# Optimization experiments

Hardware: AMD Instinct MI355X
Metric: run time of the kernel (lower is better)

The kernel has to match this reference:

```python
import jax, jax.numpy as jnp
import numpy as np


def setup_inputs() -> dict:
    key = jax.random.key(0)
    k1, k2, k3 = jax.random.split(key, 3)
    B, C, H, W = 16, 512, 64, 64
    K = 32
    std = 1.0 / (K * C) ** 0.5
    x = jax.random.normal(k1, (B, C, H, W), dtype=jnp.float32)
    codewords = jax.random.uniform(k2, (K, C), dtype=jnp.float32, minval=-std, maxval=std)
    scale = jax.random.uniform(k3, (K,), dtype=jnp.float32, minval=-1.0, maxval=0.0)
    return {"x": x, "codewords": codewords, "scale": scale}


def reference(x, codewords, scale):
    # x: [B, C, H, W] -> tokens [B, N, C] with N = H*W
    B, C, H, W = x.shape
    xf = x.reshape(B, C, H * W).transpose(0, 2, 1)  # [B, N, C]

    # (avoids materializing the [B, N, K, C] tensor the torch code builds)
    x_sq = jnp.sum(xf * xf, axis=-1)                 # [B, N]
    c_sq = jnp.sum(codewords * codewords, axis=-1)   # [K]
    xc = jnp.einsum('bnc,kc->bnk', xf, codewords)    # [B, N, K]
    scaled_l2 = scale * (x_sq[..., None] - 2.0 * xc + c_sq)  # [B, N, K]

    w = jax.nn.softmax(scaled_l2, axis=2)            # [B, N, K]

    # aggregate: sum_n w[b,n,k] * (x[b,n,:] - c[k,:])
    #          = einsum(w, x) - (sum_n w) * c
    enc = jnp.einsum('bnk,bnc->bkc', w, xf) - jnp.sum(w, axis=1)[..., None] * codewords
    return enc  # [B, K, C]
```

## Files before the change

### kernel.cpp

```cpp
#include <hip/hip_runtime.h>
#include <hip/hip_bf16.h>


#define B_ 16
#define C_ 512
#define N_ 4096
#define K_ 32
#define XCPAD 40

typedef __attribute__((ext_vector_type(8))) short short8;
typedef __attribute__((ext_vector_type(16))) float floatx16;

__device__ inline unsigned short f2bf(float f) {
    union { float f; unsigned u; } v; v.f = f;
    unsigned r = v.u + 0x7FFFu + ((v.u >> 16) & 1u);
    return (unsigned short)(r >> 16);
}

__global__ __launch_bounds__(256, 2)
void enc_kernel(const float* __restrict__ x, const float* __restrict__ cw,
                const float* __restrict__ scale, float* __restrict__ out)
{
    __shared__ unsigned short XC[C_ * XCPAD];
    __shared__ float Spart[4][32][33];
    __shared__ unsigned short Wl[K_ * XCPAD];
    __shared__ float xsqp[4][32];
    __shared__ float csq[K_];
    __shared__ float scl[K_];
    __shared__ float wsumL[K_];

    const int tid  = threadIdx.x;
    const int wave = tid >> 6;
    const int lane = tid & 63;
    const int l31  = lane & 31;
    const int lh   = lane >> 5;

    const int b     = blockIdx.x >> 5;
    const int chunk = blockIdx.x & 31;
    const long xbase = (long)b * C_ * N_;

    if (tid < K_) scl[tid] = scale[tid];
    {
        const int k = tid >> 3, p = tid & 7;
        const float4* cwr = (const float4*)(cw + k * C_ + p * 64);
        float s = 0.f;
        #pragma unroll
        for (int i = 0; i < 16; ++i) {
            float4 v = cwr[i];
            s += v.x*v.x + v.y*v.y + v.z*v.z + v.w*v.w;
        }
        s += __shfl_xor(s, 1); s += __shfl_xor(s, 2); s += __shfl_xor(s, 4);
        if (p == 0) csq[k] = s;
    }

    short8 cwf[8];
    #pragma unroll
    for (int s = 0; s < 8; ++s) {
        const float* p = cw + l31 * C_ + wave * 128 + s * 16 + lh * 8;
        short8 f;
        #pragma unroll
        for (int j = 0; j < 8; ++j) f[j] = (short)f2bf(p[j]);
        cwf[s] = f;
    }

    floatx16 acc[4];
    floatx16 accW;
    #pragma unroll
    for (int t = 0; t < 4; ++t)
        #pragma unroll
        for (int i = 0; i < 16; ++i) acc[t][i] = 0.f;
    #pragma unroll
    for (int i = 0; i < 16; ++i) accW[i] = 0.f;

    __syncthreads();

    for (int g = 0; g < 4; ++g) {
        const int n0 = chunk * 128 + g * 32;

        {
            const int c0 = tid >> 3;
            const int nq = tid & 7;
            float sq0 = 0.f, sq1 = 0.f, sq2 = 0.f, sq3 = 0.f;
            #pragma unroll
            for (int it = 0; it < 16; ++it) {
                const int c = c0 + 32 * it;
                const float4 v = *(const float4*)(x + xbase + (long)c * N_ + n0 + nq * 4);
                sq0 += v.x*v.x; sq1 += v.y*v.y; sq2 += v.z*v.z; sq3 += v.w*v.w;
                const unsigned lo = (unsigned)f2bf(v.x) | ((unsigned)f2bf(v.y) << 16);
                const unsigned hi = (unsigned)f2bf(v.z) | ((unsigned)f2bf(v.w) << 16);
                *(uint2*)&XC[c * XCPAD + nq * 4] = make_uint2(lo, hi);
            }
            #pragma unroll
            for (int m = 8; m <= 32; m <<= 1) {
                sq0 += __shfl_xor(sq0, m); sq1 += __shfl_xor(sq1, m);
                sq2 += __shfl_xor(sq2, m); sq3 += __shfl_xor(sq3, m);
            }
            if (((tid >> 3) & 7) == 0) {
                xsqp[wave][nq * 4 + 0] = sq0; xsqp[wave][nq * 4 + 1] = sq1;
                xsqp[wave][nq * 4 + 2] = sq2; xsqp[wave][nq * 4 + 3] = sq3;
            }
        }
        __syncthreads();

        {
            floatx16 S;
            #pragma unroll
            for (int i = 0; i < 16; ++i) S[i] = 0.f;
            #pragma unroll
            for (int s = 0; s < 8; ++s) {
                const int cb = wave * 128 + s * 16 + lh * 8;
                short8 a;
                #pragma unroll
                for (int j = 0; j < 8; ++j)
                    a[j] = (short)XC[(cb + j) * XCPAD + l31];
                S = __builtin_amdgcn_mfma_f32_32x32x16_bf16(a, cwf[s], S, 0, 0, 0);
            }
            #pragma unroll
            for (int r = 0; r < 16; ++r) {
                const int n = (r & 3) + 8 * (r >> 2) + 4 * lh;
                Spart[wave][n][l31] = S[r];
            }
        }
        __syncthreads();

        {
            const int n  = tid >> 3;
            const int kq = tid & 7;
            const float xq = xsqp[0][n] + xsqp[1][n] + xsqp[2][n] + xsqp[3][n];
            float L[4];
            #pragma unroll
            for (int i = 0; i < 4; ++i) {
                const int k = kq * 4 + i;
                const float s2 = Spart[0][n][k] + Spart[1][n][k]
                               + Spart[2][n][k] + Spart[3][n][k];
                L[i] = scl[k] * (xq - 2.f * s2 + csq[k]);
            }
            float m = fmaxf(fmaxf(L[0], L[1]), fmaxf(L[2], L[3]));
            m = fmaxf(m, __shfl_xor(m, 1));
            m = fmaxf(m, __shfl_xor(m, 2));
            m = fmaxf(m, __shfl_xor(m, 4));
            float e[4], sum = 0.f;
            #pragma unroll
            for (int i = 0; i < 4; ++i) { e[i] = __expf(L[i] - m); sum += e[i]; }
            sum += __shfl_xor(sum, 1); sum += __shfl_xor(sum, 2); sum += __shfl_xor(sum, 4);
            const float inv = 1.f / sum;
            #pragma unroll
            for (int i = 0; i < 4; ++i)
                Wl[(kq * 4 + i) * XCPAD + n] = f2bf(e[i] * inv);
        }
        __syncthreads();

        {
            short8 aw[2];
            #pragma unroll
            for (int sub = 0; sub < 2; ++sub)
                aw[sub] = *(const short8*)&Wl[l31 * XCPAD + sub * 16 + lh * 8];
            #pragma unroll
            for (int t4 = 0; t4 < 4; ++t4) {
                const int crow = (wave * 4 + t4) * 32 + l31;
                #pragma unroll
                for (int sub = 0; sub < 2; ++sub) {
                    const short8 bx = *(const short8*)&XC[crow * XCPAD + sub * 16 + lh * 8];
                    acc[t4] = __builtin_amdgcn_mfma_f32_32x32x16_bf16(aw[sub], bx, acc[t4], 0, 0, 0);
                }
            }
            if (wave == 0) {
                short8 ones;
                #pragma unroll
                for (int j = 0; j < 8; ++j) ones[j] = (short)0x3F80;
                #pragma unroll
                for (int sub = 0; sub < 2; ++sub)
                    accW = __builtin_amdgcn_mfma_f32_32x32x16_bf16(aw[sub], ones, accW, 0, 0, 0);
            }
        }
        __syncthreads();
    }

    if (wave == 0 && l31 == 0) {
        #pragma unroll
        for (int r = 0; r < 16; ++r) {
            const int k = (r & 3) + 8 * (r >> 2) + 4 * lh;
            wsumL[k] = accW[r];
        }
    }
    __syncthreads();

    #pragma unroll
    for (int t4 = 0; t4 < 4; ++t4) {
        const int c = (wave * 4 + t4) * 32 + l31;
        #pragma unroll
        for (int r = 0; r < 16; ++r) {
            const int k = (r & 3) + 8 * (r >> 2) + 4 * lh;
            const float val = acc[t4][r] - wsumL[k] * cw[k * C_ + c];
            atomicAdd(out + ((b * K_ + k) * C_ + c), val);
        }
    }
}

extern "C" void kernel_launch(void* const* d_in, const int* in_sizes, int n_in,
                              void* d_out, int out_size, void* d_ws, size_t ws_size,
                              hipStream_t stream) {
    const float* x     = (const float*)d_in[0];
    const float* cw    = (const float*)d_in[1];
    const float* scale = (const float*)d_in[2];
    float* out = (float*)d_out;
    hipMemsetAsync(out, 0, (size_t)out_size * sizeof(float), stream);
    hipLaunchKernelGGL(enc_kernel, dim3(B_ * 32), dim3(256), 0, stream,
                       x, cw, scale, out);
}
```

Measured before the change: 230.4 us.

## Double-buffer x loads, shrink LDS partials, and replace output atomics with workspace reduce

Global loads of x are now software-pipelined across channel quarters and groups using two register buffers, so memory latency overlaps the bf16 conversion. The per-wave Spart partials are merged through LDS atomics into a single tile, and launch bounds are raised to 3 blocks per CU. The ones-MFMA row sum is replaced by a scalar sum of the bf16 weights. When enough workspace exists, each block writes its partial result plainly and a second kernel sums the 32 chunks, replacing the memset and global atomics. The cost is an extra kernel launch plus 32 MB of workspace traffic, LDS atomic contention, and higher register pressure from the buffers.

```diff
diff --git a/kernel.cpp b/kernel.cpp
--- a/kernel.cpp
+++ b/kernel.cpp
@@ -16,13 +16,18 @@
     unsigned r = v.u + 0x7FFFu + ((v.u >> 16) & 1u);
     return (unsigned short)(r >> 16);
 }
-
-__global__ __launch_bounds__(256, 2)
+__device__ inline float bf2f(short s) {
+    union { unsigned u; float f; } v; v.u = ((unsigned)(unsigned short)s) << 16;
+    return v.f;
+}
+
+template <int USE_WS>
+__global__ __launch_bounds__(256, 3)
 void enc_kernel(const float* __restrict__ x, const float* __restrict__ cw,
-                const float* __restrict__ scale, float* __restrict__ out)
+                const float* __restrict__ scale, float* __restrict__ outp)
 {
     __shared__ unsigned short XC[C_ * XCPAD];
-    __shared__ float Spart[4][32][33];
+    __shared__ float Spart[32][33];
     __shared__ unsigned short Wl[K_ * XCPAD];
     __shared__ float xsqp[4][32];
     __shared__ float csq[K_];
@@ -40,6 +45,7 @@
     const long xbase = (long)b * C_ * N_;
 
     if (tid < K_) scl[tid] = scale[tid];
+    for (int i = tid; i < 32 * 33; i += 256) ((float*)Spart)[i] = 0.f;
     {
         const int k = tid >> 3, p = tid & 7;
         const float4* cwr = (const float4*)(cw + k * C_ + p * 64);
@@ -64,41 +70,51 @@
     }
 
     floatx16 acc[4];
-    floatx16 accW;
     #pragma unroll
     for (int t = 0; t < 4; ++t)
         #pragma unroll
         for (int i = 0; i < 16; ++i) acc[t][i] = 0.f;
-    #pragma unroll
-    for (int i = 0; i < 16; ++i) accW[i] = 0.f;
-
+    float wsum_r = 0.f;
+
+    const int c0 = tid >> 3;
+    const int nq = tid & 7;
+    const float* xg = x + xbase + (long)c0 * N_ + chunk * 128 + nq * 4;
+
+    float4 bufA[4], bufB[4];
+    #define ISSUEQ(buf, g, q)                                            \
+        { _Pragma("unroll")                                              \
+          for (int j = 0; j < 4; ++j)                                    \
+              buf[j] = *(const float4*)(xg + (long)(32 * ((q)*4 + j)) * N_ + (g) * 32); }
+
+    ISSUEQ(bufA, 0, 0);
     __syncthreads();
 
     for (int g = 0; g < 4; ++g) {
-        const int n0 = chunk * 128 + g * 32;
-
-        {
-            const int c0 = tid >> 3;
-            const int nq = tid & 7;
-            float sq0 = 0.f, sq1 = 0.f, sq2 = 0.f, sq3 = 0.f;
-            #pragma unroll
-            for (int it = 0; it < 16; ++it) {
-                const int c = c0 + 32 * it;
-                const float4 v = *(const float4*)(x + xbase + (long)c * N_ + n0 + nq * 4);
+        float sq0 = 0.f, sq1 = 0.f, sq2 = 0.f, sq3 = 0.f;
+        #pragma unroll
+        for (int q = 0; q < 4; ++q) {
+            float4* cur = (q & 1) ? bufB : bufA;
+            float4* nxt = (q & 1) ? bufA : bufB;
+            if (q < 3)      { ISSUEQ(nxt, g, q + 1); }
+            else if (g < 3) { ISSUEQ(nxt, g + 1, 0); }
+            #pragma unroll
+            for (int j = 0; j < 4; ++j) {
+                const int c = c0 + 32 * (q * 4 + j);
+                const float4 v = cur[j];
                 sq0 += v.x*v.x; sq1 += v.y*v.y; sq2 += v.z*v.z; sq3 += v.w*v.w;
                 const unsigned lo = (unsigned)f2bf(v.x) | ((unsigned)f2bf(v.y) << 16);
                 const unsigned hi = (unsigned)f2bf(v.z) | ((unsigned)f2bf(v.w) << 16);
                 *(uint2*)&XC[c * XCPAD + nq * 4] = make_uint2(lo, hi);
             }
-            #pragma unroll
-            for (int m = 8; m <= 32; m <<= 1) {
-                sq0 += __shfl_xor(sq0, m); sq1 += __shfl_xor(sq1, m);
-                sq2 += __shfl_xor(sq2, m); sq3 += __shfl_xor(sq3, m);
-            }
-            if (((tid >> 3) & 7) == 0) {
-                xsqp[wave][nq * 4 + 0] = sq0; xsqp[wave][nq * 4 + 1] = sq1;
-                xsqp[wave][nq * 4 + 2] = sq2; xsqp[wave][nq * 4 + 3] = sq3;
-            }
+        }
+        #pragma unroll
+        for (int m = 8; m <= 32; m <<= 1) {
+            sq0 += __shfl_xor(sq0, m); sq1 += __shfl_xor(sq1, m);
+            sq2 += __shfl_xor(sq2, m); sq3 += __shfl_xor(sq3, m);
+        }
+        if ((lane >> 3) == 0) {
+            xsqp[wave][nq * 4 + 0] = sq0; xsqp[wave][nq * 4 + 1] = sq1;
+            xsqp[wave][nq * 4 + 2] = sq2; xsqp[wave][nq * 4 + 3] = sq3;
         }
         __syncthreads();
 
@@ -118,7 +134,7 @@
             #pragma unroll
             for (int r = 0; r < 16; ++r) {
                 const int n = (r & 3) + 8 * (r >> 2) + 4 * lh;
-                Spart[wave][n][l31] = S[r];
+                atomicAdd(&Spart[n][l31], S[r]);
             }
         }
         __syncthreads();
@@ -131,8 +147,8 @@
             #pragma unroll
             for (int i = 0; i < 4; ++i) {
                 const int k = kq * 4 + i;
-                const float s2 = Spart[0][n][k] + Spart[1][n][k]
-                               + Spart[2][n][k] + Spart[3][n][k];
+                const float s2 = Spart[n][k];
+                Spart[n][k] = 0.f;
                 L[i] = scl[k] * (xq - 2.f * s2 + csq[k]);
             }
             float m = fmaxf(fmaxf(L[0], L[1]), fmaxf(L[2], L[3]));
@@ -155,6 +171,12 @@
             #pragma unroll
             for (int sub = 0; sub < 2; ++sub)
                 aw[sub] = *(const short8*)&Wl[l31 * XCPAD + sub * 16 + lh * 8];
+            float ws = 0.f;
+            #pragma unroll
+            for (int sub = 0; sub < 2; ++sub)
+                #pragma unroll
+                for (int j = 0; j < 8; ++j) ws += bf2f(aw[sub][j]);
+            wsum_r += ws;
             #pragma unroll
             for (int t4 = 0; t4 < 4; ++t4) {
                 const int crow = (wave * 4 + t4) * 32 + l31;
@@ -164,27 +186,16 @@
                     acc[t4] = __builtin_amdgcn_mfma_f32_32x32x16_bf16(aw[sub], bx, acc[t4], 0, 0, 0);
                 }
             }
-            if (wave == 0) {
-                short8 ones;
-                #pragma unroll
-                for (int j = 0; j < 8; ++j) ones[j] = (short)0x3F80;
-                #pragma unroll
-                for (int sub = 0; sub < 2; ++sub)
-                    accW = __builtin_amdgcn_mfma_f32_32x32x16_bf16(aw[sub], ones, accW, 0, 0, 0);
-            }
-        }
-        __syncthreads();
-    }
-
-    if (wave == 0 && l31 == 0) {
-        #pragma unroll
-        for (int r = 0; r < 16; ++r) {
-            const int k = (r & 3) + 8 * (r >> 2) + 4 * lh;
-            wsumL[k] = accW[r];
-        }
-    }
+        }
+        __syncthreads();
+    }
+
+    wsum_r += __shfl_xor(wsum_r, 32);
+    if (wave == 0 && lh == 0) wsumL[l31] = wsum_r;
     __syncthreads();
 
+    float* dst = USE_WS ? (outp + (size_t)blockIdx.x * K_ * C_)
+                        : (outp + (size_t)b * K_ * C_);
     #pragma unroll
     for (int t4 = 0; t4 < 4; ++t4) {
         const int c = (wave * 4 + t4) * 32 + l31;
@@ -192,9 +203,26 @@
         for (int r = 0; r < 16; ++r) {
             const int k = (r & 3) + 8 * (r >> 2) + 4 * lh;
             const float val = acc[t4][r] - wsumL[k] * cw[k * C_ + c];
-            atomicAdd(out + ((b * K_ + k) * C_ + c), val);
-        }
-    }
+            if (USE_WS) dst[k * C_ + c] = val;
+            else        atomicAdd(dst + k * C_ + c, val);
+        }
+    }
+}
+
+__global__ __launch_bounds__(256)
+void reduce_kernel(const float4* __restrict__ part, float4* __restrict__ out)
+{
+    const int gid = blockIdx.x * 256 + threadIdx.x;
+    const int bb  = gid >> 12;
+    const int i4  = gid & 4095;
+    const float4* p = part + ((size_t)bb * 32) * 4096 + i4;
+    float4 s = make_float4(0.f, 0.f, 0.f, 0.f);
+    #pragma unroll
+    for (int ch = 0; ch < 32; ++ch) {
+        const float4 v = p[(size_t)ch * 4096];
+        s.x += v.x; s.y += v.y; s.z += v.z; s.w += v.w;
+    }
+    out[gid] = s;
 }
 
 extern "C" void kernel_launch(void* const* d_in, const int* in_sizes, int n_in,
@@ -204,7 +232,17 @@
     const float* cw    = (const float*)d_in[1];
     const float* scale = (const float*)d_in[2];
     float* out = (float*)d_out;
-    hipMemsetAsync(out, 0, (size_t)out_size * sizeof(float), stream);
-    hipLaunchKernelGGL(enc_kernel, dim3(B_ * 32), dim3(256), 0, stream,
-                       x, cw, scale, out);
-}
+
+    const size_t ws_need = (size_t)512 * K_ * C_ * sizeof(float);
+    if (ws_size >= ws_need) {
+        float* part = (float*)d_ws;
+        hipLaunchKernelGGL(enc_kernel<1>, dim3(B_ * 32), dim3(256), 0, stream,
+                           x, cw, scale, part);
+        hipLaunchKernelGGL(reduce_kernel, dim3(256), dim3(256), 0, stream,
+                           (const float4*)part, (float4*)out);
+    } else {
+        hipMemsetAsync(out, 0, (size_t)out_size * sizeof(float), stream);
+        hipLaunchKernelGGL(enc_kernel<0>, dim3(B_ * 32), dim3(256), 0, stream,
+                           x, cw, scale, out);
+    }
+}
```

New measurement: 253.5 us. 1.1x slower.
